# Performance work log

Measured on AMD Instinct MI355X. Metric: run time of the kernel, lower is better.

The kernel has to match this reference:

```python
import jax, jax.numpy as jnp
import numpy as np

ALPHA = 1.0

def setup_inputs() -> dict:
    key = jax.random.key(0)
    k1, k2 = jax.random.split(key)
    B, T, F = 8, 4096, 1024
    x = jax.random.normal(k1, (B, T, F), dtype=jnp.float32)
    # ragged valid lengths in [T//2, T]; mask[b, t] = t < length[b]
    lengths = jax.random.randint(k2, (B,), T // 2, T + 1)
    attention_mask = (jnp.arange(T)[None, :] < lengths[:, None]).astype(jnp.int32)
    return {"input_values": x, "attention_mask": attention_mask}


def reference(input_values, attention_mask):
    # input_values: [B,T,F]; attention_mask: [B,T] (1 for valid, 0 for pad)
    m = attention_mask.astype(input_values.dtype)[..., None]          # [B,T,1]
    L = jnp.sum(m, axis=1)                                            # [B,1]
    # k: per-channel mean over valid timesteps (torch mean over dims [-1,-2])
    k = jnp.sum(input_values * m, axis=1) / L                         # [B,F]
    k_centered = k - jnp.mean(k, axis=-1, keepdims=True)              # [B,F] (center over channels)
    kd = jnp.sqrt(jnp.sum(k_centered ** 2, axis=-1, keepdims=True))   # [B,1]
    # center each timestep over channels
    x_centered = input_values - jnp.mean(input_values, axis=-1, keepdims=True)  # [B,T,F]
    qd = jnp.sqrt(jnp.sum(x_centered ** 2, axis=-1))                  # [B,T]
    num = jnp.einsum('btf,bf->bt', x_centered, k_centered)            # [B,T]
    C_qk = num / (qd * kd)                                            # [B,T]
    A = (1.0 - jax.nn.sigmoid(C_qk)) ** ALPHA                         # [B,T]
    # apply attention and zero out padded positions (original zero-pads)
    out = input_values * A[..., None] * m                             # [B,T,F]
    return out
```

## Files before the change

kernel.cpp:

```cpp
#include <hip/hip_runtime.h>
#include <math.h>

#define BB 8
#define TT 4096
#define FF 1024
#define F4 (FF / 4)
#define TS 128
#define TCHUNK (TT / TS)

typedef float vfloat4 __attribute__((ext_vector_type(4)));

__global__ __launch_bounds__(256) void k1_partial(const float4* __restrict__ x4,
                                                  const int* __restrict__ mask,
                                                  float4* __restrict__ part4,
                                                  float* __restrict__ Sk,
                                                  float* __restrict__ Skk) {
    const int ts  = blockIdx.x;
    const int b   = blockIdx.y;
    const int tid = threadIdx.x;

    if (ts == 0 && tid == 0) { Sk[b] = 0.f; Skk[b] = 0.f; }

    __shared__ int msh[TCHUNK];
    if (tid < TCHUNK) msh[tid] = mask[(size_t)b * TT + ts * TCHUNK + tid];
    __syncthreads();
    int nv = 0;
    #pragma unroll
    for (int i = 0; i < TCHUNK; ++i) nv += msh[i];
    if (nv == 0) return;

    const float4* xb = x4 + ((size_t)b * TT + (size_t)ts * TCHUNK) * F4 + tid;
    float4 acc = make_float4(0.f, 0.f, 0.f, 0.f);
    #pragma unroll 8
    for (int t = 0; t < nv; ++t) {
        float4 v = xb[(size_t)t * F4];
        acc.x += v.x; acc.y += v.y; acc.z += v.z; acc.w += v.w;
    }
    part4[((size_t)b * TS + ts) * F4 + tid] = acc;
}

__global__ __launch_bounds__(256) void k2_stats(const float* __restrict__ part,
                                                const int* __restrict__ mask,
                                                float* __restrict__ kbuf,
                                                float* __restrict__ Sk,
                                                float* __restrict__ Skk) {
    __shared__ float red[8][32];
    __shared__ float Lred[4];

    const int tid   = threadIdx.x;
    const int wave  = tid >> 6;
    const int lane  = tid & 63;
    const int b2    = blockIdx.x >> 5;
    const int fbase = (blockIdx.x & 31) * 32;

    int c = 0;
    #pragma unroll
    for (int i = 0; i < 16; ++i) c += mask[(size_t)b2 * TT + tid + 256 * i];
    float fc = (float)c;
    #pragma unroll
    for (int off = 32; off; off >>= 1) fc += __shfl_xor(fc, off);
    if (lane == 0) Lred[wave] = fc;
    __syncthreads();
    const float Lf  = Lred[0] + Lred[1] + Lred[2] + Lred[3];
    const int   nts = ((int)Lf + TCHUNK - 1) / TCHUNK;

    const int f     = fbase + (tid & 31);
    const int slice = tid >> 5;
    float s = 0.f;
    for (int t = slice; t < nts; t += 8)
        s += part[((size_t)b2 * TS + t) * FF + f];
    red[slice][tid & 31] = s;
    __syncthreads();

    if (tid < 32) {
        float sum = 0.f;
        #pragma unroll
        for (int sl = 0; sl < 8; ++sl) sum += red[sl][tid];
        const float kv = sum / Lf;
        kbuf[(size_t)b2 * FF + fbase + tid] = kv;
        float a = kv, q = kv * kv;
        #pragma unroll
        for (int off = 16; off; off >>= 1) {
            a += __shfl_xor(a, off);
            q += __shfl_xor(q, off);
        }
        if (tid == 0) {
            atomicAdd(&Sk[b2],  a);
            atomicAdd(&Skk[b2], q);
        }
    }
}

__global__ __launch_bounds__(256) void k3_apply(const float4* __restrict__ x4,
                                                const int* __restrict__ mask,
                                                const float4* __restrict__ kb4,
                                                const float* __restrict__ Sk,
                                                const float* __restrict__ Skk,
                                                float4* __restrict__ out4) {
    const int wave = threadIdx.x >> 6;
    const int lane = threadIdx.x & 63;
    const int t    = blockIdx.x * 4 + wave;
    const int b    = blockIdx.y;
    const size_t row = ((size_t)b * TT + t) * F4;

    vfloat4* orow = (vfloat4*)(out4 + row);
    if (mask[(size_t)b * TT + t] == 0) {
        vfloat4 z = (vfloat4)(0.f);
        #pragma unroll
        for (int j = 0; j < 4; ++j)
            __builtin_nontemporal_store(z, orow + lane + 64 * j);
        return;
    }

    const float4* xrow = x4 + row;
    const float4* krow = kb4 + (size_t)b * F4;
    float4 xv[4], kv[4];
    #pragma unroll
    for (int j = 0; j < 4; ++j) {
        xv[j] = xrow[lane + 64 * j];
        kv[j] = krow[lane + 64 * j];
    }

    float s1 = 0.f, s2 = 0.f, s3 = 0.f;
    #pragma unroll
    for (int j = 0; j < 4; ++j) {
        s1 += xv[j].x + xv[j].y + xv[j].z + xv[j].w;
        s2 = fmaf(xv[j].x, xv[j].x, fmaf(xv[j].y, xv[j].y,
             fmaf(xv[j].z, xv[j].z, fmaf(xv[j].w, xv[j].w, s2))));
        s3 = fmaf(xv[j].x, kv[j].x, fmaf(xv[j].y, kv[j].y,
             fmaf(xv[j].z, kv[j].z, fmaf(xv[j].w, kv[j].w, s3))));
    }
    #pragma unroll
    for (int off = 32; off; off >>= 1) {
        s1 += __shfl_xor(s1, off);
        s2 += __shfl_xor(s2, off);
        s3 += __shfl_xor(s3, off);
    }

    const float sk  = Sk[b];
    const float kd  = sqrtf(fmaxf(Skk[b] - sk * sk * (1.0f / FF), 0.f));
    const float mx  = s1 * (1.0f / FF);
    const float num = s3 - mx * sk;
    const float qd  = sqrtf(fmaxf(s2 - s1 * s1 * (1.0f / FF), 0.f));
    const float C   = num / (qd * kd);
    const float A   = 1.0f / (1.0f + __expf(C));

    #pragma unroll
    for (int j = 0; j < 4; ++j) {
        vfloat4 o;
        o.x = xv[j].x * A; o.y = xv[j].y * A;
        o.z = xv[j].z * A; o.w = xv[j].w * A;
        __builtin_nontemporal_store(o, orow + lane + 64 * j);
    }
}

extern "C" void kernel_launch(void* const* d_in, const int* in_sizes, int n_in,
                              void* d_out, int out_size, void* d_ws, size_t ws_size,
                              hipStream_t stream) {
    const float* x    = (const float*)d_in[0];
    const int*   mask = (const int*)d_in[1];
    float*       out  = (float*)d_out;

    float* part = (float*)d_ws;
    float* kbuf = part + (size_t)BB * TS * FF;
    float* Sk   = kbuf + (size_t)BB * FF;
    float* Skk  = Sk + BB;

    k1_partial<<<dim3(TS, BB), 256, 0, stream>>>((const float4*)x, mask,
                                                 (float4*)part, Sk, Skk);
    k2_stats<<<256, 256, 0, stream>>>(part, mask, kbuf, Sk, Skk);
    k3_apply<<<dim3(TT / 4, BB), 256, 0, stream>>>((const float4*)x, mask,
                                                   (const float4*)kbuf, Sk, Skk,
                                                   (float4*)out);
}
```

Baseline: 249.9 us.

## Process four rows per wave in apply kernel with prefetch; double k1 time splits

The apply kernel now gives each wave four consecutive timesteps. It loads the k vector once per wave and prefetches the next x row while reducing the current one. It reads the four mask entries with a single int4 load and zero-fills the padded rows directly. The partial-sum kernel splits time into 256 chunks instead of 128 for more parallel blocks, and reads its 16 mask values with vectorized int4 loads instead of staging them through shared memory. In exchange, the partial buffer in the workspace doubles in size and k2 must reduce more partial rows, while the apply kernel launches fewer blocks and relies on the mask being a valid-prefix layout.

```diff
diff --git a/kernel.cpp b/kernel.cpp
--- a/kernel.cpp
+++ b/kernel.cpp
@@ -5,7 +5,7 @@
 #define TT 4096
 #define FF 1024
 #define F4 (FF / 4)
-#define TS 128
+#define TS 256
 #define TCHUNK (TT / TS)
 
 typedef float vfloat4 __attribute__((ext_vector_type(4)));
@@ -21,12 +21,10 @@
 
     if (ts == 0 && tid == 0) { Sk[b] = 0.f; Skk[b] = 0.f; }
 
-    __shared__ int msh[TCHUNK];
-    if (tid < TCHUNK) msh[tid] = mask[(size_t)b * TT + ts * TCHUNK + tid];
-    __syncthreads();
-    int nv = 0;
-    #pragma unroll
-    for (int i = 0; i < TCHUNK; ++i) nv += msh[i];
+    const int4* mrow = (const int4*)(mask + (size_t)b * TT + ts * TCHUNK);
+    int4 m0 = mrow[0], m1 = mrow[1], m2 = mrow[2], m3 = mrow[3];
+    const int nv = m0.x + m0.y + m0.z + m0.w + m1.x + m1.y + m1.z + m1.w
+                 + m2.x + m2.y + m2.z + m2.w + m3.x + m3.y + m3.z + m3.w;
     if (nv == 0) return;
 
     const float4* xb = x4 + ((size_t)b * TT + (size_t)ts * TCHUNK) * F4 + tid;
@@ -99,58 +97,74 @@
                                                 float4* __restrict__ out4) {
     const int wave = threadIdx.x >> 6;
     const int lane = threadIdx.x & 63;
-    const int t    = blockIdx.x * 4 + wave;
     const int b    = blockIdx.y;
-    const size_t row = ((size_t)b * TT + t) * F4;
+    const int rowbase = blockIdx.x * 16 + wave * 4;
+    const size_t base = ((size_t)b * TT + rowbase) * F4;
 
-    vfloat4* orow = (vfloat4*)(out4 + row);
-    if (mask[(size_t)b * TT + t] == 0) {
+    const int4 m4 = *(const int4*)(mask + (size_t)b * TT + rowbase);
+    const int  nv = m4.x + m4.y + m4.z + m4.w;
+
+    for (int i = nv; i < 4; ++i) {
+        vfloat4* orow = (vfloat4*)(out4 + base + (size_t)i * F4);
         vfloat4 z = (vfloat4)(0.f);
         #pragma unroll
         for (int j = 0; j < 4; ++j)
             __builtin_nontemporal_store(z, orow + lane + 64 * j);
-        return;
     }
+    if (nv == 0) return;
 
-    const float4* xrow = x4 + row;
     const float4* krow = kb4 + (size_t)b * F4;
-    float4 xv[4], kv[4];
+    float4 kv[4];
     #pragma unroll
-    for (int j = 0; j < 4; ++j) {
-        xv[j] = xrow[lane + 64 * j];
-        kv[j] = krow[lane + 64 * j];
-    }
-
-    float s1 = 0.f, s2 = 0.f, s3 = 0.f;
-    #pragma unroll
-    for (int j = 0; j < 4; ++j) {
-        s1 += xv[j].x + xv[j].y + xv[j].z + xv[j].w;
-        s2 = fmaf(xv[j].x, xv[j].x, fmaf(xv[j].y, xv[j].y,
-             fmaf(xv[j].z, xv[j].z, fmaf(xv[j].w, xv[j].w, s2))));
-        s3 = fmaf(xv[j].x, kv[j].x, fmaf(xv[j].y, kv[j].y,
-             fmaf(xv[j].z, kv[j].z, fmaf(xv[j].w, kv[j].w, s3))));
-    }
-    #pragma unroll
-    for (int off = 32; off; off >>= 1) {
-        s1 += __shfl_xor(s1, off);
-        s2 += __shfl_xor(s2, off);
-        s3 += __shfl_xor(s3, off);
-    }
+    for (int j = 0; j < 4; ++j) kv[j] = krow[lane + 64 * j];
 
     const float sk  = Sk[b];
     const float kd  = sqrtf(fmaxf(Skk[b] - sk * sk * (1.0f / FF), 0.f));
-    const float mx  = s1 * (1.0f / FF);
-    const float num = s3 - mx * sk;
-    const float qd  = sqrtf(fmaxf(s2 - s1 * s1 * (1.0f / FF), 0.f));
-    const float C   = num / (qd * kd);
-    const float A   = 1.0f / (1.0f + __expf(C));
 
+    float4 xn[4];
     #pragma unroll
-    for (int j = 0; j < 4; ++j) {
-        vfloat4 o;
-        o.x = xv[j].x * A; o.y = xv[j].y * A;
-        o.z = xv[j].z * A; o.w = xv[j].w * A;
-        __builtin_nontemporal_store(o, orow + lane + 64 * j);
+    for (int j = 0; j < 4; ++j) xn[j] = (x4 + base)[lane + 64 * j];
+
+    for (int i = 0; i < nv; ++i) {
+        float4 xv[4];
+        #pragma unroll
+        for (int j = 0; j < 4; ++j) xv[j] = xn[j];
+        if (i + 1 < nv) {
+            const float4* xrow = x4 + base + (size_t)(i + 1) * F4;
+            #pragma unroll
+            for (int j = 0; j < 4; ++j) xn[j] = xrow[lane + 64 * j];
+        }
+
+        float s1 = 0.f, s2 = 0.f, s3 = 0.f;
+        #pragma unroll
+        for (int j = 0; j < 4; ++j) {
+            s1 += xv[j].x + xv[j].y + xv[j].z + xv[j].w;
+            s2 = fmaf(xv[j].x, xv[j].x, fmaf(xv[j].y, xv[j].y,
+                 fmaf(xv[j].z, xv[j].z, fmaf(xv[j].w, xv[j].w, s2))));
+            s3 = fmaf(xv[j].x, kv[j].x, fmaf(xv[j].y, kv[j].y,
+                 fmaf(xv[j].z, kv[j].z, fmaf(xv[j].w, kv[j].w, s3))));
+        }
+        #pragma unroll
+        for (int off = 32; off; off >>= 1) {
+            s1 += __shfl_xor(s1, off);
+            s2 += __shfl_xor(s2, off);
+            s3 += __shfl_xor(s3, off);
+        }
+
+        const float mx  = s1 * (1.0f / FF);
+        const float num = s3 - mx * sk;
+        const float qd  = sqrtf(fmaxf(s2 - s1 * s1 * (1.0f / FF), 0.f));
+        const float C   = num / (qd * kd);
+        const float A   = 1.0f / (1.0f + __expf(C));
+
+        vfloat4* orow = (vfloat4*)(out4 + base + (size_t)i * F4);
+        #pragma unroll
+        for (int j = 0; j < 4; ++j) {
+            vfloat4 o;
+            o.x = xv[j].x * A; o.y = xv[j].y * A;
+            o.z = xv[j].z * A; o.w = xv[j].w * A;
+            __builtin_nontemporal_store(o, orow + lane + 64 * j);
+        }
     }
 }
 
@@ -169,7 +183,7 @@
     k1_partial<<<dim3(TS, BB), 256, 0, stream>>>((const float4*)x, mask,
                                                  (float4*)part, Sk, Skk);
     k2_stats<<<256, 256, 0, stream>>>(part, mask, kbuf, Sk, Skk);
-    k3_apply<<<dim3(TT / 4, BB), 256, 0, stream>>>((const float4*)x, mask,
-                                                   (const float4*)kbuf, Sk, Skk,
-                                                   (float4*)out);
+    k3_apply<<<dim3(TT / 16, BB), 256, 0, stream>>>((const float4*)x, mask,
+                                                    (const float4*)kbuf, Sk, Skk,
+                                                    (float4*)out);
 }
```

Result: no change. 252.0 us (+0.8%).
